# Kernel tuning notes

Measured on AMD Instinct MI355X. Metric: run time of the kernel, lower is better.

Reference implementation:

```python
import jax, jax.numpy as jnp
import numpy as np

CHANNELS = 12
NUM_FREQ = 5
P = 1 + 2 * NUM_FREQ  # pos_embed_output_dim = 11
WORLD = (96, 96, 96)


def setup_inputs() -> dict:
    key = jax.random.key(0)
    k1, k2 = jax.random.split(key)
    xyz = jax.random.uniform(k1, (800000, 3), dtype=jnp.float32, minval=-1.0, maxval=1.0)
    # learned grid parameter [channels * P, *world_size] (torch inits zeros; use small randn for a non-trivial test)
    grid = jax.random.normal(k2, (CHANNELS * P,) + WORLD, dtype=jnp.float32) * 0.01
    xyz_min = jnp.array([-1.0, -1.0, -1.0], dtype=jnp.float32)
    xyz_max = jnp.array([1.0, 1.0, 1.0], dtype=jnp.float32)
    return {"xyz": xyz, "grid": grid, "xyz_min": xyz_min, "xyz_max": xyz_max}


def _trilinear_sample(g, coords):
    # g: [C, Dx, Dy, Dz]; coords: [N, 3] in [-1, 1] with
    # coords[:,0] -> last spatial dim Dz, coords[:,1] -> Dy, coords[:,2] -> Dx
    # (matches F.grid_sample 5D convention with align_corners=True)
    Dx, Dy, Dz = g.shape[1], g.shape[2], g.shape[3]

    def split(f, D):
        f = (f + 1.0) * 0.5 * (D - 1)  # align_corners=True mapping
        i0 = jnp.clip(jnp.floor(f).astype(jnp.int32), 0, D - 1)
        i1 = jnp.clip(i0 + 1, 0, D - 1)
        w = f - i0.astype(f.dtype)
        return i0, i1, w

    z0, z1, wz = split(coords[:, 0], Dz)
    y0, y1, wy = split(coords[:, 1], Dy)
    x0, x1, wx = split(coords[:, 2], Dx)

    def gather(ix, iy, iz):
        return g[:, ix, iy, iz]  # [C, N]

    c000 = gather(x0, y0, z0); c001 = gather(x0, y0, z1)
    c010 = gather(x0, y1, z0); c011 = gather(x0, y1, z1)
    c100 = gather(x1, y0, z0); c101 = gather(x1, y0, z1)
    c110 = gather(x1, y1, z0); c111 = gather(x1, y1, z1)

    c00 = c000 * (1 - wz) + c001 * wz
    c01 = c010 * (1 - wz) + c011 * wz
    c10 = c100 * (1 - wz) + c101 * wz
    c11 = c110 * (1 - wz) + c111 * wz
    c0 = c00 * (1 - wy) + c01 * wy
    c1 = c10 * (1 - wy) + c11 * wy
    return c0 * (1 - wx) + c1 * wx  # [C, N]


def reference(xyz, grid, xyz_min, xyz_max):
    shape = xyz.shape[:-1]
    pts = xyz.reshape(-1, 3)
    # normalize to [0,1], flip xyz -> zyx, map to [-1,1]
    ind_norm = ((pts - xyz_min) / (xyz_max - xyz_min))[:, ::-1] * 2.0 - 1.0  # [N, 3]

    freqs = 2.0 ** jnp.arange(NUM_FREQ, dtype=jnp.float32)
    comps = [ind_norm]
    for f in range(NUM_FREQ):
        comps.append(jnp.sin(freqs[f] * ind_norm))
        comps.append(jnp.cos(freqs[f] * ind_norm))
    comps = jnp.stack(comps, axis=0)  # [P, N, 3]

    grids = grid.reshape(P, CHANNELS, *WORLD)  # [P, C, Dx, Dy, Dz]
    sampled = jax.vmap(_trilinear_sample)(grids, comps)  # [P, C, N]
    out = jnp.mean(sampled, axis=0)  # [C, N]
    out = out.T.reshape(*shape, CHANNELS)  # [N, C]
    return out
```

## Files before the change

kernel.cpp:

```cpp
#include <hip/hip_runtime.h>
#include <hip/hip_fp16.h>
#include <cmath>

constexpr int D   = 96;
constexpr int C   = 12;
constexpr int P   = 11;
constexpr int VOX = D * D * D;
constexpr int CELLS = 32 * 32 * 32;

__device__ __forceinline__ unsigned spread5(unsigned v) {
  v &= 31u;
  v = (v | (v << 8)) & 0x100Fu;
  v = (v | (v << 4)) & 0x10C3u;
  v = (v | (v << 2)) & 0x1249u;
  return v;
}

__device__ __forceinline__ unsigned cell_of_u(const float u[3]) {
  unsigned cc[3];
#pragma unroll
  for (int d = 0; d < 3; ++d) {
    int c = (int)((u[d] + 1.0f) * 16.0f);
    c = c < 0 ? 0 : (c > 31 ? 31 : c);
    cc[d] = (unsigned)c;
  }
  return spread5(cc[0]) | (spread5(cc[1]) << 1) | (spread5(cc[2]) << 2);
}

__device__ __forceinline__ void norm_u(const float* __restrict__ xyz, int n,
                                       const float* __restrict__ mn,
                                       const float* __restrict__ mx, float u[3]) {
#pragma unroll
  for (int d = 0; d < 3; ++d)
    u[d] = (xyz[3 * (size_t)n + d] - mn[d]) * (2.0f / (mx[d] - mn[d])) - 1.0f;
}

__global__ __launch_bounds__(256) void transpose_count_kernel(
    const float* __restrict__ g, __half* __restrict__ gt,
    const float* __restrict__ xyz, const float* __restrict__ mn,
    const float* __restrict__ mx, unsigned* __restrict__ counts, int N) {
  constexpr int RPT = VOX / 4;
  int t = blockIdx.x * 256 + threadIdx.x;

  if (t < P * RPT) {
    int p = t / RPT;
    int r4 = (t - p * RPT) * 4;
    const float* src = g + (size_t)p * C * VOX + r4;
    float4 v[C];
#pragma unroll
    for (int c = 0; c < C; ++c)
      v[c] = *reinterpret_cast<const float4*>(src + (size_t)c * VOX);
    union { __half h[48]; uint4 u[6]; } pk;
#pragma unroll
    for (int j = 0; j < 4; ++j) {
#pragma unroll
      for (int c = 0; c < C; ++c) {
        float f = (j == 0) ? v[c].x : (j == 1) ? v[c].y : (j == 2) ? v[c].z : v[c].w;
        pk.h[j * C + c] = __float2half_rn(f);
      }
    }
    uint4* dst = reinterpret_cast<uint4*>(gt + ((size_t)p * VOX + r4) * C);
#pragma unroll
    for (int k = 0; k < 6; ++k) dst[k] = pk.u[k];
  }

  if (t < N) {
    float u[3];
    norm_u(xyz, t, mn, mx, u);
    atomicAdd(&counts[cell_of_u(u)], 1u);
  }
}

__global__ __launch_bounds__(1024) void scan_kernel(
    const unsigned* __restrict__ counts, unsigned* __restrict__ offsets) {
  __shared__ unsigned part[1024];
  int t = threadIdx.x;
  unsigned base = t * (CELLS / 1024);
  unsigned local[CELLS / 1024];
  unsigned s = 0;
#pragma unroll
  for (int i = 0; i < CELLS / 1024; ++i) { local[i] = s; s += counts[base + i]; }
  part[t] = s;
  __syncthreads();
  for (int off = 1; off < 1024; off <<= 1) {
    unsigned v = (t >= off) ? part[t - off] : 0u;
    __syncthreads();
    part[t] += v;
    __syncthreads();
  }
  unsigned prev = (t == 0) ? 0u : part[t - 1];
#pragma unroll
  for (int i = 0; i < CELLS / 1024; ++i) offsets[base + i] = prev + local[i];
}

__global__ __launch_bounds__(256) void scatter_kernel(
    const float* __restrict__ xyz, const float* __restrict__ mn,
    const float* __restrict__ mx, unsigned* __restrict__ offsets,
    float4* __restrict__ sorted, int N) {
  int n = blockIdx.x * 256 + threadIdx.x;
  if (n >= N) return;
  float u[3];
  norm_u(xyz, n, mn, mx, u);
  unsigned slot = atomicAdd(&offsets[cell_of_u(u)], 1u);
  float4 rec;
  rec.x = u[0]; rec.y = u[1]; rec.z = u[2];
  rec.w = __uint_as_float((unsigned)n);
  sorted[slot] = rec;
}

__global__ __launch_bounds__(256) void sample_sorted_kernel(
    const float4* __restrict__ pts, const __half* __restrict__ g,
    float* __restrict__ out, int N) {
  unsigned nwg = gridDim.x, bid = blockIdx.x;
  unsigned q = nwg / 8u, r = nwg % 8u;
  unsigned xcd = bid % 8u, j = bid / 8u;
  unsigned swz = (xcd < r ? xcd * (q + 1u) : r * (q + 1u) + (xcd - r) * q) + j;
  int n = (int)(swz * 256u + threadIdx.x);
  if (n >= N) return;

  float4 rec = pts[n];

  float acc[C];
#pragma unroll
  for (int c = 0; c < C; ++c) acc[c] = 0.0f;

  const char* gb = reinterpret_cast<const char*>(g);
  unsigned pbase = 0u;

  auto gather = [&](float ex, float ey, float ez) {
    float tz = fmaf(ez, 47.5f, 47.5f);
    float ty = fmaf(ey, 47.5f, 47.5f);
    float tx = fmaf(ex, 47.5f, 47.5f);
    float fz = floorf(tz), fy = floorf(ty), fx = floorf(tx);
    int z0 = (int)fz, y0 = (int)fy, x0 = (int)fx;
    int y1 = y0 + 1 > D - 1 ? D - 1 : y0 + 1;
    int x1 = x0 + 1 > D - 1 ? D - 1 : x0 + 1;
    float wz1 = tz - fz, wz0 = 1.0f - wz1;
    float wy1 = ty - fy, wy0 = 1.0f - wy1;
    float wx1 = tx - fx, wx0 = 1.0f - wx1;

    auto consume = [&](const uint4& q0, const uint4& q1, const uint4& q2,
                       float wxy) {
      float w0 = wxy * wz0, w1 = wxy * wz1;
      auto acc2 = [&](unsigned lo, unsigned hi, int c) {
        __half2 hl = *reinterpret_cast<const __half2*>(&lo);
        __half2 hh = *reinterpret_cast<const __half2*>(&hi);
        float2 f0 = __half22float2(hl);
        float2 f1 = __half22float2(hh);
        acc[c]     = fmaf(w0, f0.x, fmaf(w1, f1.x, acc[c]));
        acc[c + 1] = fmaf(w0, f0.y, fmaf(w1, f1.y, acc[c + 1]));
      };
      acc2(q0.x, q1.z, 0);
      acc2(q0.y, q1.w, 2);
      acc2(q0.z, q2.x, 4);
      acc2(q0.w, q2.y, 6);
      acc2(q1.x, q2.z, 8);
      acc2(q1.y, q2.w, 10);
    };

    unsigned bx0 = (unsigned)(x0 * (D * D) + z0);
    unsigned bx1 = (unsigned)(x1 * (D * D) + z0);
    unsigned by0 = (unsigned)(y0 * D), by1 = (unsigned)(y1 * D);

    unsigned o = pbase + (bx0 + by0) * 24u;
    uint4 a0 = *reinterpret_cast<const uint4*>(gb + o);
    uint4 a1 = *reinterpret_cast<const uint4*>(gb + o + 16);
    uint4 a2 = *reinterpret_cast<const uint4*>(gb + o + 32);
    o = pbase + (bx0 + by1) * 24u;
    uint4 b0 = *reinterpret_cast<const uint4*>(gb + o);
    uint4 b1 = *reinterpret_cast<const uint4*>(gb + o + 16);
    uint4 b2 = *reinterpret_cast<const uint4*>(gb + o + 32);

    consume(a0, a1, a2, wx0 * wy0);

    o = pbase + (bx1 + by0) * 24u;
    a0 = *reinterpret_cast<const uint4*>(gb + o);
    a1 = *reinterpret_cast<const uint4*>(gb + o + 16);
    a2 = *reinterpret_cast<const uint4*>(gb + o + 32);

    consume(b0, b1, b2, wx0 * wy1);

    o = pbase + (bx1 + by1) * 24u;
    b0 = *reinterpret_cast<const uint4*>(gb + o);
    b1 = *reinterpret_cast<const uint4*>(gb + o + 16);
    b2 = *reinterpret_cast<const uint4*>(gb + o + 32);

    consume(a0, a1, a2, wx1 * wy0);
    consume(b0, b1, b2, wx1 * wy1);

    pbase += (unsigned)VOX * 24u;
  };

  gather(rec.x, rec.y, rec.z);

  float s0 = sinf(rec.x), c0_ = cosf(rec.x);
  float s1 = sinf(rec.y), c1_ = cosf(rec.y);
  float s2 = sinf(rec.z), c2_ = cosf(rec.z);
  for (int f = 0; f < 5; ++f) {
    gather(s0, s1, s2);
    gather(c0_, c1_, c2_);
    if (f < 4) {
      float ns;
      ns = 2.0f * s0 * c0_; c0_ = 1.0f - 2.0f * s0 * s0; s0 = ns;
      ns = 2.0f * s1 * c1_; c1_ = 1.0f - 2.0f * s1 * s1; s1 = ns;
      ns = 2.0f * s2 * c2_; c2_ = 1.0f - 2.0f * s2 * s2; s2 = ns;
    }
  }

  constexpr float inv = 1.0f / (float)P;
  float4 r0, r1, r2;
  r0.x = acc[0] * inv;  r0.y = acc[1] * inv;  r0.z = acc[2] * inv;  r0.w = acc[3] * inv;
  r1.x = acc[4] * inv;  r1.y = acc[5] * inv;  r1.z = acc[6] * inv;  r1.w = acc[7] * inv;
  r2.x = acc[8] * inv;  r2.y = acc[9] * inv;  r2.z = acc[10] * inv; r2.w = acc[11] * inv;
  unsigned oidx = __float_as_uint(rec.w);
  float4* o4 = reinterpret_cast<float4*>(out + (size_t)oidx * C);
  o4[0] = r0; o4[1] = r1; o4[2] = r2;
}

__global__ __launch_bounds__(256) void sample_fp16_kernel(
    const float* __restrict__ xyz, const __half* __restrict__ g,
    const float* __restrict__ xyz_min, const float* __restrict__ xyz_max,
    float* __restrict__ out, int N) {
  int n = blockIdx.x * 256 + threadIdx.x;
  if (n >= N) return;
  float u[3];
#pragma unroll
  for (int d = 0; d < 3; ++d) {
    float mn = xyz_min[d], mx = xyz_max[d];
    u[d] = (xyz[3 * (size_t)n + d] - mn) * (2.0f / (mx - mn)) - 1.0f;
  }
  float acc[C];
#pragma unroll
  for (int c = 0; c < C; ++c) acc[c] = 0.0f;
  const ushort* gu = reinterpret_cast<const ushort*>(g);
  int p = 0;
  auto gather = [&](float ex, float ey, float ez) {
    float tz = (ez + 1.0f) * (0.5f * (D - 1));
    float ty = (ey + 1.0f) * (0.5f * (D - 1));
    float tx = (ex + 1.0f) * (0.5f * (D - 1));
    int z0 = (int)floorf(tz); z0 = z0 < 0 ? 0 : (z0 > D - 1 ? D - 1 : z0);
    int y0 = (int)floorf(ty); y0 = y0 < 0 ? 0 : (y0 > D - 1 ? D - 1 : y0);
    int x0 = (int)floorf(tx); x0 = x0 < 0 ? 0 : (x0 > D - 1 ? D - 1 : x0);
    int y1 = y0 + 1 > D - 1 ? D - 1 : y0 + 1;
    int x1 = x0 + 1 > D - 1 ? D - 1 : x0 + 1;
    float wz = tz - (float)z0, wy = ty - (float)y0, wx = tx - (float)x0;
    float wz0 = 1.0f - wz, wz1 = wz;
    float wy0 = 1.0f - wy, wy1 = wy;
    float wx0 = 1.0f - wx, wx1 = wx;
    size_t pbase = (size_t)p * VOX;
    const uint4* r00 = reinterpret_cast<const uint4*>(gu + (pbase + (size_t)((x0 * D + y0) * D + z0)) * C);
    const uint4* r01 = reinterpret_cast<const uint4*>(gu + (pbase + (size_t)((x0 * D + y1) * D + z0)) * C);
    const uint4* r10 = reinterpret_cast<const uint4*>(gu + (pbase + (size_t)((x1 * D + y0) * D + z0)) * C);
    const uint4* r11 = reinterpret_cast<const uint4*>(gu + (pbase + (size_t)((x1 * D + y1) * D + z0)) * C);
    uint4 a0 = r00[0], a1 = r00[1], a2 = r00[2];
    uint4 b0 = r01[0], b1 = r01[1], b2 = r01[2];
    uint4 c0 = r10[0], c1 = r10[1], c2 = r10[2];
    uint4 d0 = r11[0], d1 = r11[1], d2 = r11[2];
    auto acc2 = [&](unsigned lo, unsigned hi, float w0, float w1, int c) {
      __half2 hl = *reinterpret_cast<const __half2*>(&lo);
      __half2 hh = *reinterpret_cast<const __half2*>(&hi);
      float2 f0 = __half22float2(hl);
      float2 f1 = __half22float2(hh);
      acc[c]     = fmaf(w0, f0.x, fmaf(w1, f1.x, acc[c]));
      acc[c + 1] = fmaf(w0, f0.y, fmaf(w1, f1.y, acc[c + 1]));
    };
    auto region = [&](const uint4& q0, const uint4& q1, const uint4& q2, float wxy) {
      float w0 = wxy * wz0, w1 = wxy * wz1;
      acc2(q0.x, q1.z, w0, w1, 0);
      acc2(q0.y, q1.w, w0, w1, 2);
      acc2(q0.z, q2.x, w0, w1, 4);
      acc2(q0.w, q2.y, w0, w1, 6);
      acc2(q1.x, q2.z, w0, w1, 8);
      acc2(q1.y, q2.w, w0, w1, 10);
    };
    region(a0, a1, a2, wx0 * wy0);
    region(b0, b1, b2, wx0 * wy1);
    region(c0, c1, c2, wx1 * wy0);
    region(d0, d1, d2, wx1 * wy1);
    ++p;
  };
  gather(u[0], u[1], u[2]);
  float s[3], co[3];
#pragma unroll
  for (int d = 0; d < 3; ++d) { s[d] = sinf(u[d]); co[d] = cosf(u[d]); }
  for (int f = 0; f < 5; ++f) {
    gather(s[0], s[1], s[2]);
    gather(co[0], co[1], co[2]);
    if (f < 4) {
#pragma unroll
      for (int d = 0; d < 3; ++d) {
        float ns = 2.0f * s[d] * co[d];
        float nc = 1.0f - 2.0f * s[d] * s[d];
        s[d] = ns; co[d] = nc;
      }
    }
  }
  constexpr float inv = 1.0f / (float)P;
  float4 r0, r1, r2;
  r0.x = acc[0] * inv;  r0.y = acc[1] * inv;  r0.z = acc[2] * inv;  r0.w = acc[3] * inv;
  r1.x = acc[4] * inv;  r1.y = acc[5] * inv;  r1.z = acc[6] * inv;  r1.w = acc[7] * inv;
  r2.x = acc[8] * inv;  r2.y = acc[9] * inv;  r2.z = acc[10] * inv; r2.w = acc[11] * inv;
  float4* o4 = reinterpret_cast<float4*>(out + (size_t)n * C);
  o4[0] = r0; o4[1] = r1; o4[2] = r2;
}

__global__ __launch_bounds__(256) void sample_naive_kernel(
    const float* __restrict__ xyz, const float* __restrict__ g,
    const float* __restrict__ xyz_min, const float* __restrict__ xyz_max,
    float* __restrict__ out, int N) {
  int n = blockIdx.x * 256 + threadIdx.x;
  if (n >= N) return;
  float u[3];
#pragma unroll
  for (int d = 0; d < 3; ++d) {
    float mn = xyz_min[d], mx = xyz_max[d];
    u[d] = (xyz[3 * (size_t)n + d] - mn) * (2.0f / (mx - mn)) - 1.0f;
  }
  float acc[C];
#pragma unroll
  for (int c = 0; c < C; ++c) acc[c] = 0.0f;
  int p = 0;
  auto gather = [&](float ex, float ey, float ez) {
    float e[3] = {ez, ey, ex};
    int i0[3], i1[3]; float w[3];
#pragma unroll
    for (int d = 0; d < 3; ++d) {
      float t = (e[d] + 1.0f) * (0.5f * (D - 1));
      int a = (int)floorf(t);
      a = a < 0 ? 0 : (a > D - 1 ? D - 1 : a);
      int b = a + 1 > D - 1 ? D - 1 : a + 1;
      i0[d] = a; i1[d] = b; w[d] = t - (float)a;
    }
    const float* gp = g + (size_t)p * C * VOX;
    auto corner = [&](int iz, int iy, int ix, float wgt) {
      int o = (ix * D + iy) * D + iz;
#pragma unroll
      for (int c = 0; c < C; ++c) acc[c] += wgt * gp[(size_t)c * VOX + o];
    };
    corner(i0[0], i0[1], i0[2], (1 - w[0]) * (1 - w[1]) * (1 - w[2]));
    corner(i1[0], i0[1], i0[2], w[0] * (1 - w[1]) * (1 - w[2]));
    corner(i0[0], i1[1], i0[2], (1 - w[0]) * w[1] * (1 - w[2]));
    corner(i1[0], i1[1], i0[2], w[0] * w[1] * (1 - w[2]));
    corner(i0[0], i0[1], i1[2], (1 - w[0]) * (1 - w[1]) * w[2]);
    corner(i1[0], i0[1], i1[2], w[0] * (1 - w[1]) * w[2]);
    corner(i0[0], i1[1], i1[2], (1 - w[0]) * w[1] * w[2]);
    corner(i1[0], i1[1], i1[2], w[0] * w[1] * w[2]);
    ++p;
  };
  gather(u[0], u[1], u[2]);
  float s[3], co[3];
#pragma unroll
  for (int d = 0; d < 3; ++d) { s[d] = sinf(u[d]); co[d] = cosf(u[d]); }
  for (int f = 0; f < 5; ++f) {
    gather(s[0], s[1], s[2]);
    gather(co[0], co[1], co[2]);
    if (f < 4) {
#pragma unroll
      for (int d = 0; d < 3; ++d) {
        float ns = 2.0f * s[d] * co[d];
        float nc = 1.0f - 2.0f * s[d] * s[d];
        s[d] = ns; co[d] = nc;
      }
    }
  }
  constexpr float inv = 1.0f / (float)P;
#pragma unroll
  for (int c = 0; c < C; ++c) out[(size_t)n * C + c] = acc[c] * inv;
}

extern "C" void kernel_launch(void* const* d_in, const int* in_sizes, int n_in,
                              void* d_out, int out_size, void* d_ws, size_t ws_size,
                              hipStream_t stream) {
  const float* xyz = (const float*)d_in[0];
  const float* grid = (const float*)d_in[1];
  const float* mn = (const float*)d_in[2];
  const float* mx = (const float*)d_in[3];
  float* out = (float*)d_out;
  int N = in_sizes[0] / 3;

  size_t gt_bytes = (size_t)P * VOX * C * sizeof(__half);
  size_t sorted_bytes = (size_t)N * sizeof(float4);
  size_t cnt_bytes = (size_t)CELLS * sizeof(unsigned);

  size_t need_sorted = sorted_bytes + gt_bytes + 2 * cnt_bytes + 1024;
  size_t need_min = gt_bytes + 256;

  int sblocks = (N + 255) / 256;
  int tblocks = (P * (VOX / 4) + 255) / 256;

  if (ws_size >= need_sorted) {
    char* w = (char*)d_ws;
    float4*   sorted  = (float4*)w;   w += sorted_bytes;
    __half*   gt      = (__half*)w;   w += gt_bytes;
    unsigned* counts  = (unsigned*)w; w += cnt_bytes;
    unsigned* offsets = (unsigned*)w;

    hipMemsetAsync(counts, 0, cnt_bytes, stream);
    transpose_count_kernel<<<tblocks, 256, 0, stream>>>(grid, gt, xyz, mn, mx,
                                                        counts, N);
    scan_kernel<<<1, 1024, 0, stream>>>(counts, offsets);
    scatter_kernel<<<sblocks, 256, 0, stream>>>(xyz, mn, mx, offsets, sorted, N);
    sample_sorted_kernel<<<sblocks, 256, 0, stream>>>(sorted, gt, out, N);
  } else if (ws_size >= need_min) {
    __half* gt = (__half*)d_ws;
    transpose_count_kernel<<<tblocks, 256, 0, stream>>>(grid, gt, xyz, mn, mx,
                                                        nullptr, 0);
    sample_fp16_kernel<<<sblocks, 256, 0, stream>>>(xyz, gt, mn, mx, out, N);
  } else {
    sample_naive_kernel<<<sblocks, 256, 0, stream>>>(xyz, grid, mn, mx, out, N);
  }
}
```

Measured before the change: 567.8 us.

## Split sorted sampling into four passes over embedding-component subsets

Replaces the single sorted-sample kernel with four templated launches, each gathering from only 2-3 of the 11 positional-embedding grids. Partial sums go to an fp32 workspace buffer, and the last pass applies the mean and scatters to the original point order. The goal is a per-pass working set (about 3 grids × 21 MB of fp16) that fits better in L2/MALL cache than all 11 grids touched at once. It also issues three corner loads before the first consume, for more memory-level parallelism. The cost is extra launches and extra global read/write traffic on the partial-sum buffer, plus a larger workspace requirement that could push execution onto a fallback path.

```diff
diff --git a/kernel.cpp b/kernel.cpp
--- a/kernel.cpp
+++ b/kernel.cpp
@@ -108,9 +108,10 @@
   sorted[slot] = rec;
 }
 
-__global__ __launch_bounds__(256) void sample_sorted_kernel(
+template <int PSTART, int PCNT, int MODE>
+__global__ __launch_bounds__(256) void sample_pass_kernel(
     const float4* __restrict__ pts, const __half* __restrict__ g,
-    float* __restrict__ out, int N) {
+    float* __restrict__ outw, float* __restrict__ out, int N) {
   unsigned nwg = gridDim.x, bid = blockIdx.x;
   unsigned q = nwg / 8u, r = nwg % 8u;
   unsigned xcd = bid % 8u, j = bid / 8u;
@@ -125,7 +126,7 @@
   for (int c = 0; c < C; ++c) acc[c] = 0.0f;
 
   const char* gb = reinterpret_cast<const char*>(g);
-  unsigned pbase = 0u;
+  unsigned pbase = (unsigned)PSTART * (unsigned)VOX * 24u;
 
   auto gather = [&](float ex, float ey, float ez) {
     float tz = fmaf(ez, 47.5f, 47.5f);
@@ -170,51 +171,79 @@
     uint4 b0 = *reinterpret_cast<const uint4*>(gb + o);
     uint4 b1 = *reinterpret_cast<const uint4*>(gb + o + 16);
     uint4 b2 = *reinterpret_cast<const uint4*>(gb + o + 32);
+    o = pbase + (bx1 + by0) * 24u;
+    uint4 c0 = *reinterpret_cast<const uint4*>(gb + o);
+    uint4 c1 = *reinterpret_cast<const uint4*>(gb + o + 16);
+    uint4 c2 = *reinterpret_cast<const uint4*>(gb + o + 32);
 
     consume(a0, a1, a2, wx0 * wy0);
 
-    o = pbase + (bx1 + by0) * 24u;
+    o = pbase + (bx1 + by1) * 24u;
     a0 = *reinterpret_cast<const uint4*>(gb + o);
     a1 = *reinterpret_cast<const uint4*>(gb + o + 16);
     a2 = *reinterpret_cast<const uint4*>(gb + o + 32);
 
     consume(b0, b1, b2, wx0 * wy1);
-
-    o = pbase + (bx1 + by1) * 24u;
-    b0 = *reinterpret_cast<const uint4*>(gb + o);
-    b1 = *reinterpret_cast<const uint4*>(gb + o + 16);
-    b2 = *reinterpret_cast<const uint4*>(gb + o + 32);
-
-    consume(a0, a1, a2, wx1 * wy0);
-    consume(b0, b1, b2, wx1 * wy1);
+    consume(c0, c1, c2, wx1 * wy0);
+    consume(a0, a1, a2, wx1 * wy1);
 
     pbase += (unsigned)VOX * 24u;
   };
 
-  gather(rec.x, rec.y, rec.z);
-
-  float s0 = sinf(rec.x), c0_ = cosf(rec.x);
-  float s1 = sinf(rec.y), c1_ = cosf(rec.y);
-  float s2 = sinf(rec.z), c2_ = cosf(rec.z);
-  for (int f = 0; f < 5; ++f) {
-    gather(s0, s1, s2);
-    gather(c0_, c1_, c2_);
-    if (f < 4) {
-      float ns;
-      ns = 2.0f * s0 * c0_; c0_ = 1.0f - 2.0f * s0 * s0; s0 = ns;
-      ns = 2.0f * s1 * c1_; c1_ = 1.0f - 2.0f * s1 * s1; s1 = ns;
-      ns = 2.0f * s2 * c2_; c2_ = 1.0f - 2.0f * s2 * s2; s2 = ns;
+  float sx = sinf(rec.x), cxv = cosf(rec.x);
+  float sy = sinf(rec.y), cyv = cosf(rec.y);
+  float sz = sinf(rec.z), czv = cosf(rec.z);
+  int curj = 0;
+
+#pragma unroll
+  for (int i = 0; i < PCNT; ++i) {
+    const int comp = PSTART + i;
+    float ex, ey, ez;
+    if (comp == 0) {
+      ex = rec.x; ey = rec.y; ez = rec.z;
+    } else {
+      const int jf = (comp - 1) >> 1;
+      const bool is_cos = ((comp - 1) & 1);
+      while (curj < jf) {
+        float ns;
+        ns = 2.0f * sx * cxv; cxv = 1.0f - 2.0f * sx * sx; sx = ns;
+        ns = 2.0f * sy * cyv; cyv = 1.0f - 2.0f * sy * sy; sy = ns;
+        ns = 2.0f * sz * czv; czv = 1.0f - 2.0f * sz * sz; sz = ns;
+        ++curj;
+      }
+      ex = is_cos ? cxv : sx;
+      ey = is_cos ? cyv : sy;
+      ez = is_cos ? czv : sz;
     }
-  }
-
-  constexpr float inv = 1.0f / (float)P;
-  float4 r0, r1, r2;
-  r0.x = acc[0] * inv;  r0.y = acc[1] * inv;  r0.z = acc[2] * inv;  r0.w = acc[3] * inv;
-  r1.x = acc[4] * inv;  r1.y = acc[5] * inv;  r1.z = acc[6] * inv;  r1.w = acc[7] * inv;
-  r2.x = acc[8] * inv;  r2.y = acc[9] * inv;  r2.z = acc[10] * inv; r2.w = acc[11] * inv;
-  unsigned oidx = __float_as_uint(rec.w);
-  float4* o4 = reinterpret_cast<float4*>(out + (size_t)oidx * C);
-  o4[0] = r0; o4[1] = r1; o4[2] = r2;
+    gather(ex, ey, ez);
+  }
+
+  float4* w4 = reinterpret_cast<float4*>(outw + (size_t)n * C);
+  if (MODE == 0) {
+    float4 r0, r1, r2;
+    r0.x = acc[0]; r0.y = acc[1]; r0.z = acc[2];  r0.w = acc[3];
+    r1.x = acc[4]; r1.y = acc[5]; r1.z = acc[6];  r1.w = acc[7];
+    r2.x = acc[8]; r2.y = acc[9]; r2.z = acc[10]; r2.w = acc[11];
+    w4[0] = r0; w4[1] = r1; w4[2] = r2;
+  } else if (MODE == 1) {
+    float4 r0 = w4[0], r1 = w4[1], r2 = w4[2];
+    r0.x += acc[0]; r0.y += acc[1]; r0.z += acc[2];  r0.w += acc[3];
+    r1.x += acc[4]; r1.y += acc[5]; r1.z += acc[6];  r1.w += acc[7];
+    r2.x += acc[8]; r2.y += acc[9]; r2.z += acc[10]; r2.w += acc[11];
+    w4[0] = r0; w4[1] = r1; w4[2] = r2;
+  } else {
+    constexpr float inv = 1.0f / (float)P;
+    float4 r0 = w4[0], r1 = w4[1], r2 = w4[2];
+    r0.x = (r0.x + acc[0]) * inv;  r0.y = (r0.y + acc[1]) * inv;
+    r0.z = (r0.z + acc[2]) * inv;  r0.w = (r0.w + acc[3]) * inv;
+    r1.x = (r1.x + acc[4]) * inv;  r1.y = (r1.y + acc[5]) * inv;
+    r1.z = (r1.z + acc[6]) * inv;  r1.w = (r1.w + acc[7]) * inv;
+    r2.x = (r2.x + acc[8]) * inv;  r2.y = (r2.y + acc[9]) * inv;
+    r2.z = (r2.z + acc[10]) * inv; r2.w = (r2.w + acc[11]) * inv;
+    unsigned oidx = __float_as_uint(rec.w);
+    float4* o4 = reinterpret_cast<float4*>(out + (size_t)oidx * C);
+    o4[0] = r0; o4[1] = r1; o4[2] = r2;
+  }
 }
 
 __global__ __launch_bounds__(256) void sample_fp16_kernel(
@@ -380,18 +409,20 @@
 
   size_t gt_bytes = (size_t)P * VOX * C * sizeof(__half);
   size_t sorted_bytes = (size_t)N * sizeof(float4);
+  size_t outw_bytes = (size_t)N * C * sizeof(float);
   size_t cnt_bytes = (size_t)CELLS * sizeof(unsigned);
 
-  size_t need_sorted = sorted_bytes + gt_bytes + 2 * cnt_bytes + 1024;
+  size_t need_pass = sorted_bytes + gt_bytes + outw_bytes + 2 * cnt_bytes + 1024;
   size_t need_min = gt_bytes + 256;
 
   int sblocks = (N + 255) / 256;
   int tblocks = (P * (VOX / 4) + 255) / 256;
 
-  if (ws_size >= need_sorted) {
+  if (ws_size >= need_pass) {
     char* w = (char*)d_ws;
     float4*   sorted  = (float4*)w;   w += sorted_bytes;
     __half*   gt      = (__half*)w;   w += gt_bytes;
+    float*    outw    = (float*)w;    w += outw_bytes;
     unsigned* counts  = (unsigned*)w; w += cnt_bytes;
     unsigned* offsets = (unsigned*)w;
 
@@ -400,7 +431,10 @@
                                                         counts, N);
     scan_kernel<<<1, 1024, 0, stream>>>(counts, offsets);
     scatter_kernel<<<sblocks, 256, 0, stream>>>(xyz, mn, mx, offsets, sorted, N);
-    sample_sorted_kernel<<<sblocks, 256, 0, stream>>>(sorted, gt, out, N);
+    sample_pass_kernel<0, 3, 0><<<sblocks, 256, 0, stream>>>(sorted, gt, outw, out, N);
+    sample_pass_kernel<3, 3, 1><<<sblocks, 256, 0, stream>>>(sorted, gt, outw, out, N);
+    sample_pass_kernel<6, 3, 1><<<sblocks, 256, 0, stream>>>(sorted, gt, outw, out, N);
+    sample_pass_kernel<9, 2, 2><<<sblocks, 256, 0, stream>>>(sorted, gt, outw, out, N);
   } else if (ws_size >= need_min) {
     __half* gt = (__half*)d_ws;
     transpose_count_kernel<<<tblocks, 256, 0, stream>>>(grid, gt, xyz, mn, mx,
```

Measured after the change: 800.2 us. +40.9%, slower.
